# Kernel optimization log

Hardware: AMD Instinct MI355X
Metric: run time of the kernel (lower is better)

## Reference

```python
import jax, jax.numpy as jnp
import numpy as np

TEMPERATURE = 8.0  # sqrt(head_dim=64)
NEG_BIG = -10000.0


def setup_inputs() -> dict:
    key = jax.random.key(0)
    kq, kk, kv, km = jax.random.split(key, 4)
    B, H, S, D, K = 4, 8, 1024, 64, 4
    q = jax.random.normal(kq, (B, H, S, D), dtype=jnp.float32)
    k = jax.random.normal(kk, (B, H, S, D), dtype=jnp.float32)
    v = jax.random.normal(kv, (B, H, S, D), dtype=jnp.float32)
    # K binary attention masks, broadcastable to [B,H,S,S]
    mask = jax.random.randint(km, (K, 1, 1, S, S), 0, 2).astype(jnp.float32)
    return {"q": q, "k": k, "v": v, "mask": mask}


def reference(q, k, v, mask):
    # attn: [B,H,S,S]
    attn = jnp.einsum("bhsd,bhtd->bhst", q / TEMPERATURE, k)
    # additive mask: [K,1,1,S,S]
    ext_mask = (1.0 - mask) * NEG_BIG
    # batched over K instead of the original python loop: [K,B,H,S,S]
    probs = jax.nn.softmax(attn[None] + ext_mask, axis=-1)
    # dropout is identity in eval mode (deterministic reference)
    output = jnp.einsum("kbhst,bhtd->kbhsd", probs, v)
    return (output, attn)
```

## Files before the change

kernel.cpp:

```cpp
#include <hip/hip_runtime.h>
#include <hip/hip_bf16.h>
#include <stdint.h>

typedef float f4 __attribute__((ext_vector_type(4)));
typedef short bf8 __attribute__((ext_vector_type(8)));
typedef uint32_t u4 __attribute__((ext_vector_type(4)));
typedef uint32_t u2 __attribute__((ext_vector_type(2)));

#define SDIM 1024
#define DDIM 64
#define NBH  32
#define KM   4
#define NT   16

#define MB_BLK 4096
#define KB_BLK 1024
#define VT_BLK 512

__device__ __forceinline__ unsigned short f2bf(float f) {
  uint32_t u = __builtin_bit_cast(uint32_t, f);
  u += 0x7fffu + ((u >> 16) & 1u);
  return (unsigned short)(u >> 16);
}

#define GLOAD16(gsrc, ldst)                                                  \
  __builtin_amdgcn_global_load_lds(                                          \
      (const __attribute__((address_space(1))) unsigned int*)(gsrc),         \
      (__attribute__((address_space(3))) unsigned int*)(ldst), 16, 0, 0)

__device__ __forceinline__ bf8 lds_ld(const unsigned short* base, int row, int e0) {
  return *(const bf8*)((const char*)base + (((row * 64 + e0) * 2) ^ ((row & 7) << 4)));
}

__global__ __launch_bounds__(256) void prepass(
    const float* __restrict__ k, const float* __restrict__ v,
    const float* __restrict__ mask, unsigned short* __restrict__ kb,
    unsigned short* __restrict__ vt, uint32_t* __restrict__ mb2) {
  __shared__ float tv[64][65];
  const int b = blockIdx.x;
  const int t = threadIdx.x;
  if (b < MB_BLK) {
    int gid4 = (b * 256 + t) * 4;
    f4 x = *(const f4*)(mask + gid4);
    uint32_t bits = (x[0] > 0.5f ? 1u : 0u) | (x[1] > 0.5f ? 2u : 0u) |
                    (x[2] > 0.5f ? 4u : 0u) | (x[3] > 0.5f ? 8u : 0u);
    uint32_t wv = bits << (gid4 & 28);
    wv |= __shfl_xor(wv, 1);
    wv |= __shfl_xor(wv, 2);
    wv |= __shfl_xor(wv, 4);
    if ((t & 7) == 0) {
      int m = gid4 >> 20;
      int r = (gid4 >> 10) & 1023;
      int c = gid4 & 1023;
      mb2[m * 32768 + (c >> 5) * 1024 + r] = wv;
    }
  } else if (b < MB_BLK + KB_BLK) {
    int base = ((b - MB_BLK) * 256 + t) * 8;
    f4 a = *(const f4*)(k + base);
    f4 c = *(const f4*)(k + base + 4);
    bf8 o;
    o[0] = (short)f2bf(a[0]); o[1] = (short)f2bf(a[1]);
    o[2] = (short)f2bf(a[2]); o[3] = (short)f2bf(a[3]);
    o[4] = (short)f2bf(c[0]); o[5] = (short)f2bf(c[1]);
    o[6] = (short)f2bf(c[2]); o[7] = (short)f2bf(c[3]);
    *(bf8*)(kb + base) = o;
  } else {
    int vb = b - MB_BLK - KB_BLK;
    int bh = vb >> 4;
    int s0 = (vb & 15) * 64;
    int sr = t >> 2, c0 = (t & 3) * 16;
    const float* vp = v + ((size_t)(bh * SDIM) + s0 + sr) * DDIM + c0;
#pragma unroll
    for (int i = 0; i < 4; ++i) {
      f4 x = *(const f4*)(vp + 4 * i);
#pragma unroll
      for (int j = 0; j < 4; ++j) tv[sr][c0 + 4 * i + j] = x[j];
    }
    __syncthreads();
    int d = t >> 2, sc0 = (t & 3) * 16;
    unsigned short tmp[16];
#pragma unroll
    for (int i = 0; i < 16; ++i) tmp[i] = f2bf(tv[sc0 + i][d]);
    unsigned short* op = vt + ((size_t)(bh * DDIM) + d) * SDIM + s0 + sc0;
    bf8 o0, o1;
#pragma unroll
    for (int j = 0; j < 8; ++j) { o0[j] = (short)tmp[j]; o1[j] = (short)tmp[j + 8]; }
    *(bf8*)(op) = o0;
    *(bf8*)(op + 8) = o1;
  }
}

__global__ __launch_bounds__(512, 4) void attn_main(
    const float* __restrict__ qf, const unsigned short* __restrict__ kb,
    const unsigned short* __restrict__ vtg, const uint32_t* __restrict__ mb2,
    float* __restrict__ outO, float* __restrict__ attn) {
  __shared__ __align__(16) unsigned short k_s0[64 * 64];
  __shared__ __align__(16) unsigned short k_s1[64 * 64];
  __shared__ __align__(16) unsigned short v_s0[64 * 64];
  __shared__ __align__(16) unsigned short v_s1[64 * 64];
  __shared__ __align__(16) unsigned short e_s[64 * 64];

  const int tid = threadIdx.x;
  const int l   = tid & 63;
  const int w   = tid >> 6;
  const int l16 = l & 15;
  const int lg  = l >> 4;
  const int rt  = w >> 1;
  const int cp  = w & 1;

  int bid = (int)blockIdx.x;
  bid = (bid & 7) * 64 + (bid >> 3);
  const int bh = bid >> 4;
  const int r0 = (bid & 15) * 64;

  const int srow = tid >> 3;
  const int sd   = ((tid & 7) ^ (srow & 7)) << 3;
  const unsigned short* ksrc = kb  + ((size_t)(bh * SDIM) + srow) * DDIM + sd;
  const unsigned short* vsrc = vtg + ((size_t)(bh * DDIM) + srow) * SDIM + sd;

  GLOAD16(ksrc, k_s0 + tid * 8);
  GLOAD16(vsrc, v_s0 + tid * 8);

  bf8 bq0, bq1;
  {
    const float* qp = qf + ((size_t)(bh * SDIM) + r0 + 16 * rt + l16) * DDIM + lg * 8;
    f4 a0 = *(const f4*)qp;
    f4 a1 = *(const f4*)(qp + 4);
    f4 a2 = *(const f4*)(qp + 32);
    f4 a3 = *(const f4*)(qp + 36);
#pragma unroll
    for (int j = 0; j < 4; ++j) {
      bq0[j]     = (short)f2bf(a0[j] * 0.125f);
      bq0[j + 4] = (short)f2bf(a1[j] * 0.125f);
      bq1[j]     = (short)f2bf(a2[j] * 0.125f);
      bq1[j + 4] = (short)f2bf(a3[j] * 0.125f);
    }
  }

  f4 acc[2][4] = {};
  f4 accl[2]   = {};
  bf8 ones;
#pragma unroll
  for (int b = 0; b < 8; ++b) ones[b] = (short)0x3F80;

  const uint32_t* mbase = mb2 + rt * 32768 + r0 + l16;

  uint32_t mdwA[2][2], mdwB[2][2];
#pragma unroll
  for (int mt2 = 0; mt2 < 2; ++mt2)
#pragma unroll
    for (int kt = 0; kt < 2; ++kt)
      mdwA[mt2][kt] = mbase[kt * 1024 + 32 * cp + 16 * mt2];

  __syncthreads();

#define BODY(CT, KR, VR, KW, VW, MR, MW, PF)                                   \
  {                                                                            \
             \
    if (PF) {                                                                  \
      GLOAD16(ksrc + (size_t)((CT) + 1) * 4096, (KW) + tid * 8);               \
      GLOAD16(vsrc + (size_t)((CT) + 1) * 64, (VW) + tid * 8);                 \
      _Pragma("unroll") for (int mt2 = 0; mt2 < 2; ++mt2)                      \
        _Pragma("unroll") for (int kt = 0; kt < 2; ++kt)                       \
          (MW)[mt2][kt] = mbase[(((CT) + 1) * 2 + kt) * 1024 + 32 * cp + 16 * mt2]; \
    }                                                                          \
    f4 s0 = {}, s1 = {};                                                       \
    {                                                                          \
      const int kc0 = 32 * cp + l16;                                           \
      bf8 ak0 = lds_ld((KR), kc0, lg * 8);                                     \
      bf8 ak1 = lds_ld((KR), kc0, lg * 8 + 32);                                \
      bf8 ak2 = lds_ld((KR), kc0 + 16, lg * 8);                                \
      bf8 ak3 = lds_ld((KR), kc0 + 16, lg * 8 + 32);                           \
      s0 = __builtin_amdgcn_mfma_f32_16x16x32_bf16(ak0, bq0, s0, 0, 0, 0);     \
      s0 = __builtin_amdgcn_mfma_f32_16x16x32_bf16(ak1, bq1, s0, 0, 0, 0);     \
      s1 = __builtin_amdgcn_mfma_f32_16x16x32_bf16(ak2, bq0, s1, 0, 0, 0);     \
      s1 = __builtin_amdgcn_mfma_f32_16x16x32_bf16(ak3, bq1, s1, 0, 0, 0);     \
      const int erow = 16 * rt + l16;                                          \
      u2 ev0, ev1;                                                             \
      ev0[0] = (uint32_t)f2bf(__expf(s0[0])) | ((uint32_t)f2bf(__expf(s0[1])) << 16); \
      ev0[1] = (uint32_t)f2bf(__expf(s0[2])) | ((uint32_t)f2bf(__expf(s0[3])) << 16); \
      ev1[0] = (uint32_t)f2bf(__expf(s1[0])) | ((uint32_t)f2bf(__expf(s1[1])) << 16); \
      ev1[1] = (uint32_t)f2bf(__expf(s1[2])) | ((uint32_t)f2bf(__expf(s1[3])) << 16); \
      const int colA = 32 * cp + 4 * lg;                                       \
      *(u2*)((char*)e_s + (((erow * 64 + colA) * 2) ^ ((erow & 7) << 4))) = ev0; \
      *(u2*)((char*)e_s + (((erow * 64 + colA + 16) * 2) ^ ((erow & 7) << 4))) = ev1; \
    }                                                                          \
    asm volatile("s_waitcnt lgkmcnt(0)\n\ts_barrier" ::: "memory");            \
    {                                                                          \
                  \
      float* arow = attn + ((size_t)(bh * SDIM) + r0 + 16 * rt + l16) * SDIM   \
                    + (CT) * 64 + 32 * cp + 4 * lg;                            \
      *(f4*)(arow) = s0;                                                       \
      *(f4*)(arow + 16) = s1;                                                  \
      bf8 af[2][2];                                                            \
      _Pragma("unroll") for (int mt2 = 0; mt2 < 2; ++mt2) {                    \
        const int row = 32 * cp + 16 * mt2 + l16;                              \
        _Pragma("unroll") for (int kt = 0; kt < 2; ++kt) {                     \
          bf8 e = lds_ld(e_s, row, kt * 32 + lg * 8);                          \
          uint32_t bits = ((MR)[mt2][kt] >> (lg * 8)) & 0xffu;                 \
          u4 ew = __builtin_bit_cast(u4, e);                                   \
          _Pragma("unroll") for (int d = 0; d < 4; ++d) {                      \
            uint32_t n2 = (bits >> (2 * d)) & 3u;                              \
            uint32_t sp = (n2 * 0x8001u) & 0x00010001u;                        \
            ew[d] &= (sp << 16) - sp;                                          \
          }                                                                    \
          af[mt2][kt] = __builtin_bit_cast(bf8, ew);                           \
        }                                                                      \
        accl[mt2] = __builtin_amdgcn_mfma_f32_16x16x32_bf16(af[mt2][0], ones, accl[mt2], 0, 0, 0); \
        accl[mt2] = __builtin_amdgcn_mfma_f32_16x16x32_bf16(af[mt2][1], ones, accl[mt2], 0, 0, 0); \
      }                                                                        \
      _Pragma("unroll") for (int nt = 0; nt < 4; ++nt) {                       \
        const int dc = 16 * nt + l16;                                          \
        bf8 bv0 = lds_ld((VR), dc, lg * 8);                                    \
        bf8 bv1 = lds_ld((VR), dc, lg * 8 + 32);                               \
        _Pragma("unroll") for (int mt2 = 0; mt2 < 2; ++mt2) {                  \
          acc[mt2][nt] = __builtin_amdgcn_mfma_f32_16x16x32_bf16(af[mt2][0], bv0, acc[mt2][nt], 0, 0, 0); \
          acc[mt2][nt] = __builtin_amdgcn_mfma_f32_16x16x32_bf16(af[mt2][1], bv1, acc[mt2][nt], 0, 0, 0); \
        }                                                                      \
      }                                                                        \
    }                                                                          \
    asm volatile("s_waitcnt vmcnt(2) lgkmcnt(0)\n\ts_barrier" ::: "memory");   \
  }

  for (int ct2 = 0; ct2 < NT / 2; ++ct2) {
    BODY(2 * ct2,     k_s0, v_s0, k_s1, v_s1, mdwA, mdwB, true);
    BODY(2 * ct2 + 1, k_s1, v_s1, k_s0, v_s0, mdwB, mdwA, (ct2 < NT / 2 - 1));
  }
#undef BODY

#pragma unroll
  for (int mt2 = 0; mt2 < 2; ++mt2) {
#pragma unroll
    for (int r = 0; r < 4; ++r) {
      float inv = 1.0f / accl[mt2][r];
      int row = 32 * cp + 16 * mt2 + 4 * lg + r;
      float* orow = outO + (((size_t)(rt * NBH + bh)) * SDIM + r0 + row) * DDIM + l16;
#pragma unroll
      for (int nt = 0; nt < 4; ++nt)
        orow[16 * nt] = acc[mt2][nt][r] * inv;
    }
  }
}

extern "C" void kernel_launch(void* const* d_in, const int* in_sizes, int n_in,
                              void* d_out, int out_size, void* d_ws, size_t ws_size,
                              hipStream_t stream) {
  (void)in_sizes; (void)n_in; (void)out_size; (void)ws_size;
  const float* q    = (const float*)d_in[0];
  const float* k    = (const float*)d_in[1];
  const float* v    = (const float*)d_in[2];
  const float* mask = (const float*)d_in[3];
  float* outO = (float*)d_out;
  float* attn = (float*)d_out + (size_t)KM * NBH * SDIM * DDIM;

  char* ws = (char*)d_ws;
  unsigned short* kb = (unsigned short*)ws;
  unsigned short* vt = (unsigned short*)(ws + (4u << 20));
  uint32_t*       mb = (uint32_t*)(ws + (8u << 20));

  prepass<<<MB_BLK + KB_BLK + VT_BLK, 256, 0, stream>>>(k, v, mask, kb, vt, mb);
  attn_main<<<NBH * 16, 512, 0, stream>>>(q, kb, vt, mb, outO, attn);
}
```

Before: 57.64 us.

## Software-pipeline QK^T of the next tile with PV of the current tile

Restructures the main loop so that each iteration computes QK^T, exp and the attn store for tile t+1 while doing the masked PV and row-sum MFMAs for tile t. The exp scratch buffer is double-buffered, and K is prefetched two tiles ahead. This removes one of the two block barriers per tile and lets the VALU exp work interleave with the PV matrix ops. In exchange it uses more LDS and registers, and the end-of-iteration barrier becomes a full __syncthreads, which may wait on every outstanding global transfer.

```diff
diff --git a/kernel.cpp b/kernel.cpp
--- a/kernel.cpp
+++ b/kernel.cpp
@@ -98,7 +98,8 @@
   __shared__ __align__(16) unsigned short k_s1[64 * 64];
   __shared__ __align__(16) unsigned short v_s0[64 * 64];
   __shared__ __align__(16) unsigned short v_s1[64 * 64];
-  __shared__ __align__(16) unsigned short e_s[64 * 64];
+  __shared__ __align__(16) unsigned short e_s0[64 * 64];
+  __shared__ __align__(16) unsigned short e_s1[64 * 64];
 
   const int tid = threadIdx.x;
   const int l   = tid & 63;
@@ -118,8 +119,9 @@
   const unsigned short* ksrc = kb  + ((size_t)(bh * SDIM) + srow) * DDIM + sd;
   const unsigned short* vsrc = vtg + ((size_t)(bh * DDIM) + srow) * SDIM + sd;
 
-  GLOAD16(ksrc, k_s0 + tid * 8);
-  GLOAD16(vsrc, v_s0 + tid * 8);
+  GLOAD16(ksrc,        k_s0 + tid * 8);
+  GLOAD16(ksrc + 4096, k_s1 + tid * 8);
+  GLOAD16(vsrc,        v_s0 + tid * 8);
 
   bf8 bq0, bq1;
   {
@@ -154,50 +156,48 @@
 
   __syncthreads();
 
-#define BODY(CT, KR, VR, KW, VW, MR, MW, PF)                                   \
+#define QKSTEP(CT, KN, EN)                                                     \
   {                                                                            \
-             \
-    if (PF) {                                                                  \
-      GLOAD16(ksrc + (size_t)((CT) + 1) * 4096, (KW) + tid * 8);               \
-      GLOAD16(vsrc + (size_t)((CT) + 1) * 64, (VW) + tid * 8);                 \
-      _Pragma("unroll") for (int mt2 = 0; mt2 < 2; ++mt2)                      \
-        _Pragma("unroll") for (int kt = 0; kt < 2; ++kt)                       \
-          (MW)[mt2][kt] = mbase[(((CT) + 1) * 2 + kt) * 1024 + 32 * cp + 16 * mt2]; \
-    }                                                                          \
+    const int kc0 = 32 * cp + l16;                                             \
+    bf8 ak0 = lds_ld((KN), kc0, lg * 8);                                       \
+    bf8 ak1 = lds_ld((KN), kc0, lg * 8 + 32);                                  \
+    bf8 ak2 = lds_ld((KN), kc0 + 16, lg * 8);                                  \
+    bf8 ak3 = lds_ld((KN), kc0 + 16, lg * 8 + 32);                             \
     f4 s0 = {}, s1 = {};                                                       \
+    s0 = __builtin_amdgcn_mfma_f32_16x16x32_bf16(ak0, bq0, s0, 0, 0, 0);       \
+    s0 = __builtin_amdgcn_mfma_f32_16x16x32_bf16(ak1, bq1, s0, 0, 0, 0);       \
+    s1 = __builtin_amdgcn_mfma_f32_16x16x32_bf16(ak2, bq0, s1, 0, 0, 0);       \
+    s1 = __builtin_amdgcn_mfma_f32_16x16x32_bf16(ak3, bq1, s1, 0, 0, 0);       \
+    float* arow = attn + ((size_t)(bh * SDIM) + r0 + 16 * rt + l16) * SDIM     \
+                  + (CT) * 64 + 32 * cp + 4 * lg;                              \
+    *(f4*)(arow) = s0;                                                         \
+    *(f4*)(arow + 16) = s1;                                                    \
+    const int erow = 16 * rt + l16;                                            \
+    u2 ev0, ev1;                                                               \
+    ev0[0] = (uint32_t)f2bf(__expf(s0[0])) | ((uint32_t)f2bf(__expf(s0[1])) << 16); \
+    ev0[1] = (uint32_t)f2bf(__expf(s0[2])) | ((uint32_t)f2bf(__expf(s0[3])) << 16); \
+    ev1[0] = (uint32_t)f2bf(__expf(s1[0])) | ((uint32_t)f2bf(__expf(s1[1])) << 16); \
+    ev1[1] = (uint32_t)f2bf(__expf(s1[2])) | ((uint32_t)f2bf(__expf(s1[3])) << 16); \
+    const int colA = 32 * cp + 4 * lg;                                         \
+    *(u2*)((char*)(EN) + (((erow * 64 + colA) * 2) ^ ((erow & 7) << 4))) = ev0; \
+    *(u2*)((char*)(EN) + (((erow * 64 + colA + 16) * 2) ^ ((erow & 7) << 4))) = ev1; \
+  }
+
+  QKSTEP(0, k_s0, e_s0)
+  asm volatile("s_waitcnt lgkmcnt(0)\n\ts_barrier" ::: "memory");
+
+#define BODY(CT, KN, VC, KW, VW, EC, EN, MC, MN, QKF, PFK, PFV)                \
+  {                                                                            \
+    if (PFK) GLOAD16(ksrc + (size_t)((CT) + 2) * 4096, (KW) + tid * 8);        \
+    if (PFV) GLOAD16(vsrc + (size_t)((CT) + 1) * 64, (VW) + tid * 8);          \
+    if (QKF) QKSTEP((CT) + 1, KN, EN)                                          \
     {                                                                          \
-      const int kc0 = 32 * cp + l16;                                           \
-      bf8 ak0 = lds_ld((KR), kc0, lg * 8);                                     \
-      bf8 ak1 = lds_ld((KR), kc0, lg * 8 + 32);                                \
-      bf8 ak2 = lds_ld((KR), kc0 + 16, lg * 8);                                \
-      bf8 ak3 = lds_ld((KR), kc0 + 16, lg * 8 + 32);                           \
-      s0 = __builtin_amdgcn_mfma_f32_16x16x32_bf16(ak0, bq0, s0, 0, 0, 0);     \
-      s0 = __builtin_amdgcn_mfma_f32_16x16x32_bf16(ak1, bq1, s0, 0, 0, 0);     \
-      s1 = __builtin_amdgcn_mfma_f32_16x16x32_bf16(ak2, bq0, s1, 0, 0, 0);     \
-      s1 = __builtin_amdgcn_mfma_f32_16x16x32_bf16(ak3, bq1, s1, 0, 0, 0);     \
-      const int erow = 16 * rt + l16;                                          \
-      u2 ev0, ev1;                                                             \
-      ev0[0] = (uint32_t)f2bf(__expf(s0[0])) | ((uint32_t)f2bf(__expf(s0[1])) << 16); \
-      ev0[1] = (uint32_t)f2bf(__expf(s0[2])) | ((uint32_t)f2bf(__expf(s0[3])) << 16); \
-      ev1[0] = (uint32_t)f2bf(__expf(s1[0])) | ((uint32_t)f2bf(__expf(s1[1])) << 16); \
-      ev1[1] = (uint32_t)f2bf(__expf(s1[2])) | ((uint32_t)f2bf(__expf(s1[3])) << 16); \
-      const int colA = 32 * cp + 4 * lg;                                       \
-      *(u2*)((char*)e_s + (((erow * 64 + colA) * 2) ^ ((erow & 7) << 4))) = ev0; \
-      *(u2*)((char*)e_s + (((erow * 64 + colA + 16) * 2) ^ ((erow & 7) << 4))) = ev1; \
-    }                                                                          \
-    asm volatile("s_waitcnt lgkmcnt(0)\n\ts_barrier" ::: "memory");            \
-    {                                                                          \
-                  \
-      float* arow = attn + ((size_t)(bh * SDIM) + r0 + 16 * rt + l16) * SDIM   \
-                    + (CT) * 64 + 32 * cp + 4 * lg;                            \
-      *(f4*)(arow) = s0;                                                       \
-      *(f4*)(arow + 16) = s1;                                                  \
       bf8 af[2][2];                                                            \
       _Pragma("unroll") for (int mt2 = 0; mt2 < 2; ++mt2) {                    \
         const int row = 32 * cp + 16 * mt2 + l16;                              \
         _Pragma("unroll") for (int kt = 0; kt < 2; ++kt) {                     \
-          bf8 e = lds_ld(e_s, row, kt * 32 + lg * 8);                          \
-          uint32_t bits = ((MR)[mt2][kt] >> (lg * 8)) & 0xffu;                 \
+          bf8 e = lds_ld((EC), row, kt * 32 + lg * 8);                         \
+          uint32_t bits = ((MC)[mt2][kt] >> (lg * 8)) & 0xffu;                 \
           u4 ew = __builtin_bit_cast(u4, e);                                   \
           _Pragma("unroll") for (int d = 0; d < 4; ++d) {                      \
             uint32_t n2 = (bits >> (2 * d)) & 3u;                              \
@@ -211,22 +211,31 @@
       }                                                                        \
       _Pragma("unroll") for (int nt = 0; nt < 4; ++nt) {                       \
         const int dc = 16 * nt + l16;                                          \
-        bf8 bv0 = lds_ld((VR), dc, lg * 8);                                    \
-        bf8 bv1 = lds_ld((VR), dc, lg * 8 + 32);                               \
+        bf8 bv0 = lds_ld((VC), dc, lg * 8);                                    \
+        bf8 bv1 = lds_ld((VC), dc, lg * 8 + 32);                               \
         _Pragma("unroll") for (int mt2 = 0; mt2 < 2; ++mt2) {                  \
           acc[mt2][nt] = __builtin_amdgcn_mfma_f32_16x16x32_bf16(af[mt2][0], bv0, acc[mt2][nt], 0, 0, 0); \
           acc[mt2][nt] = __builtin_amdgcn_mfma_f32_16x16x32_bf16(af[mt2][1], bv1, acc[mt2][nt], 0, 0, 0); \
         }                                                                      \
       }                                                                        \
     }                                                                          \
-    asm volatile("s_waitcnt vmcnt(2) lgkmcnt(0)\n\ts_barrier" ::: "memory");   \
+    if (QKF) {                                                                 \
+      _Pragma("unroll") for (int mt2 = 0; mt2 < 2; ++mt2)                      \
+        _Pragma("unroll") for (int kt = 0; kt < 2; ++kt)                       \
+          (MN)[mt2][kt] = mbase[(((CT) + 1) * 2 + kt) * 1024 + 32 * cp + 16 * mt2]; \
+    }                                                                          \
+    __syncthreads();                                                           \
   }
 
   for (int ct2 = 0; ct2 < NT / 2; ++ct2) {
-    BODY(2 * ct2,     k_s0, v_s0, k_s1, v_s1, mdwA, mdwB, true);
-    BODY(2 * ct2 + 1, k_s1, v_s1, k_s0, v_s0, mdwB, mdwA, (ct2 < NT / 2 - 1));
+    const bool lastp = (ct2 == NT / 2 - 1);
+    BODY(2 * ct2,     k_s1, v_s0, k_s0, v_s1, e_s0, e_s1, mdwA, mdwB,
+         true, !lastp, true)
+    BODY(2 * ct2 + 1, k_s0, v_s1, k_s1, v_s0, e_s1, e_s0, mdwB, mdwA,
+         !lastp, !lastp, !lastp)
   }
 #undef BODY
+#undef QKSTEP
 
 #pragma unroll
   for (int mt2 = 0; mt2 < 2; ++mt2) {
```

Result: faster. 53.47 us (median of 4 runs) (-7.2%).
